# Optimization experiments

Measured on AMD Instinct MI355X. Metric: run time of the kernel, lower is better.

Reference implementation:

```python
import jax, jax.numpy as jnp
import numpy as np

N = 10000   # nodes (cells)
E = 100000  # edges
G = 2000    # num_genes
H = 20      # heads
C1 = 128    # layer-1 out channels per head
C2 = 128    # latent_dim
NEG_SLOPE = 0.2


def setup_inputs():
    key = jax.random.key(0)
    ks = jax.random.split(key, 9)
    s = 0.05
    return {
        "x": jax.random.normal(ks[0], (N, G), jnp.float32),
        "edge_index": jax.random.randint(ks[1], (2, E), 0, N, dtype=jnp.int64),
        "W1": jax.random.normal(ks[2], (G, H * C1), jnp.float32) * s,
        "att_src1": jax.random.normal(ks[3], (H, C1), jnp.float32) * s,
        "att_dst1": jax.random.normal(ks[4], (H, C1), jnp.float32) * s,
        "b1": jnp.zeros((H * C1,), jnp.float32),
        "W2": jax.random.normal(ks[5], (H * C1, H * C2), jnp.float32) * s,
        "att_src2": jax.random.normal(ks[6], (H, C2), jnp.float32) * s,
        "att_dst2": jax.random.normal(ks[7], (H, C2), jnp.float32) * s,
        "b2": jnp.zeros((C2,), jnp.float32),
    }


def _gat_conv(x, W, att_src, att_dst, bias, src, dst, concat):
    """PyG GATConv (eval mode, self-loops already in src/dst)."""
    n = x.shape[0]
    h_, c_ = att_src.shape
    h = (x @ W).reshape(n, h_, c_)                      # [N, H, C]
    a_src = jnp.einsum("nhc,hc->nh", h, att_src)        # [N, H]
    a_dst = jnp.einsum("nhc,hc->nh", h, att_dst)        # [N, H]
    e = a_src[src] + a_dst[dst]                          # [E, H]
    e = jnp.where(e > 0, e, NEG_SLOPE * e)               # leaky_relu
    # segment softmax over incoming edges of each destination node
    e_max = jax.ops.segment_max(e, dst, num_segments=n)  # [N, H]
    ex = jnp.exp(e - e_max[dst])                         # [E, H]
    denom = jax.ops.segment_sum(ex, dst, num_segments=n)
    alpha = ex / denom[dst]                              # [E, H]
    msg = alpha[:, :, None] * h[src]                     # [E, H, C]
    out = jax.ops.segment_sum(msg, dst, num_segments=n)  # [N, H, C]
    if concat:
        out = out.reshape(n, h_ * c_)
    else:
        out = out.mean(axis=1)                           # [N, C]
    return out + bias


def reference(x, edge_index, W1, att_src1, att_dst1, b1, W2, att_src2, att_dst2, b2):
    n = x.shape[0]
    loop = jnp.arange(n, dtype=edge_index.dtype)
    src = jnp.concatenate([edge_index[0], loop])  # PyG add_self_loops=True
    dst = jnp.concatenate([edge_index[1], loop])
    h1 = _gat_conv(x, W1, att_src1, att_dst1, b1, src, dst, concat=True)
    h1 = jax.nn.relu(h1)  # dropout is identity in eval mode
    h2 = _gat_conv(h1, W2, att_src2, att_dst2, b2, src, dst, concat=False)
    return jax.nn.relu(h2)
```

## Files before the change

### kernel.cpp

```cpp
#include <hip/hip_runtime.h>

#define NEG_SLOPE 0.2f

typedef __attribute__((ext_vector_type(4))) float floatx4;
typedef __attribute__((ext_vector_type(8))) short shortx8;

__device__ __forceinline__ unsigned short f2bf(float f) {
  union { float f; unsigned int u; } v;
  v.f = f;
  unsigned int r = (v.u + 0x7FFFu + ((v.u >> 16) & 1u)) >> 16;
  return (unsigned short)r;
}
__device__ __forceinline__ float bf2f(unsigned short u) {
  union { unsigned int u; float f; } v;
  v.u = (unsigned int)u << 16;
  return v.f;
}
__device__ __forceinline__ void store_out(float* p, float v) { *p = v; }
__device__ __forceinline__ void store_out(unsigned short* p, float v) { *p = f2bf(v); }

__device__ __forceinline__ void gload_lds16(const unsigned short* g, unsigned short* l) {
  __builtin_amdgcn_global_load_lds(
      (const __attribute__((address_space(1))) void*)(g),
      (__attribute__((address_space(3))) void*)(l), 16, 0, 0);
}

__device__ __forceinline__ int load_edge(const void* ei, long idx, int is64) {
  if (is64) return (int)((const long long*)ei)[idx];
  return ((const int*)ei)[idx];
}

__global__ void detect64_kernel(const unsigned int* __restrict__ p, int* __restrict__ flag) {
  int is64 = 1;
  for (int i = 0; i < 32; ++i)
    if (p[2 * i + 1] != 0u) is64 = 0;
  *flag = is64;
}

__global__ void init_cnt_kernel(int* __restrict__ cnt, int n) {
  int i = blockIdx.x * blockDim.x + threadIdx.x;
  if (i < n) cnt[i] = 1;
}

__global__ void count_kernel(const void* __restrict__ ei, const int* __restrict__ flag, int E,
                             int* __restrict__ cnt) {
  int e = blockIdx.x * blockDim.x + threadIdx.x;
  if (e >= E) return;
  int is64 = *flag;
  int d = load_edge(ei, (long)E + e, is64);
  atomicAdd(&cnt[d], 1);
}

__global__ __launch_bounds__(1024) void scan_kernel(const int* __restrict__ cnt,
                                                    int* __restrict__ offs, int n) {
  __shared__ int partial[1024];
  int t = threadIdx.x;
  int per = (n + 1023) / 1024;
  int beg = t * per;
  int end = min(beg + per, n);
  int sum = 0;
  for (int i = beg; i < end; ++i) sum += cnt[i];
  partial[t] = sum;
  __syncthreads();
  for (int d = 1; d < 1024; d <<= 1) {
    int v = (t >= d) ? partial[t - d] : 0;
    __syncthreads();
    partial[t] += v;
    __syncthreads();
  }
  int excl = (t == 0) ? 0 : partial[t - 1];
  for (int i = beg; i < end; ++i) { offs[i] = excl; excl += cnt[i]; }
  if (t == 1023) offs[n] = partial[1023];
}

__global__ void init_self_kernel(const int* __restrict__ offs, int* __restrict__ srcs,
                                 int* __restrict__ fill, int n) {
  int i = blockIdx.x * blockDim.x + threadIdx.x;
  if (i < n) { srcs[offs[i]] = i; fill[i] = 1; }
}

__global__ void scatter_kernel(const void* __restrict__ ei, const int* __restrict__ flag, int E,
                               const int* __restrict__ offs, int* __restrict__ fill,
                               int* __restrict__ srcs) {
  int e = blockIdx.x * blockDim.x + threadIdx.x;
  if (e >= E) return;
  int is64 = *flag;
  int s = load_edge(ei, e, is64);
  int d = load_edge(ei, (long)E + e, is64);
  int pos = offs[d] + atomicAdd(&fill[d], 1);
  srcs[pos] = s;
}


__global__ __launch_bounds__(256) void pack_a_kernel(const float* __restrict__ in,
                                                     unsigned short* __restrict__ out, int M,
                                                     int K, int Kpad) {
  int rt = blockIdx.x;
  int r = threadIdx.x & 127;
  int kq = threadIdx.x >> 7;
  int row = rt * 128 + r;
  int nkc = Kpad >> 3;
  unsigned short* obase = out + (long)rt * Kpad * 128 + r * 8;
  const float* irow = in + (long)row * K;
  for (int kc = kq + (int)blockIdx.y * 2; kc < nkc; kc += (int)gridDim.y * 2) {
    int k = kc << 3;
    shortx8 o;
    if (row < M && k + 8 <= K && (K & 3) == 0) {
      float4 v0 = *(const float4*)(irow + k);
      float4 v1 = *(const float4*)(irow + k + 4);
      o[0] = (short)f2bf(v0.x); o[1] = (short)f2bf(v0.y);
      o[2] = (short)f2bf(v0.z); o[3] = (short)f2bf(v0.w);
      o[4] = (short)f2bf(v1.x); o[5] = (short)f2bf(v1.y);
      o[6] = (short)f2bf(v1.z); o[7] = (short)f2bf(v1.w);
    } else {
#pragma unroll
      for (int i = 0; i < 8; ++i) {
        int kk = k + i;
        float v = (row < M && kk < K) ? irow[kk] : 0.f;
        o[i] = (short)f2bf(v);
      }
    }
    *(shortx8*)(obase + (long)kc * 1024) = o;
  }
}

__global__ __launch_bounds__(256) void transpose_pack_kernel(const float* __restrict__ in,
                                                             unsigned short* __restrict__ out,
                                                             int K, int N, int Kpad) {
  __shared__ float tile[32][33];
  int kb = blockIdx.x * 32;
  int nb = blockIdx.y * 32;
  int tx = threadIdx.x & 31;
  int ty = threadIdx.x >> 5;
#pragma unroll
  for (int i = 0; i < 32; i += 8) {
    int k = kb + ty + i;
    tile[ty + i][tx] = (k < K) ? in[(long)k * N + nb + tx] : 0.f;
  }
  __syncthreads();
  if (threadIdx.x < 128) {
    int nl = threadIdx.x & 31;
    int nn = nb + nl;
    int kc4 = threadIdx.x >> 5;
    int k0 = kc4 * 8;
    shortx8 o;
#pragma unroll
    for (int j = 0; j < 8; ++j) o[j] = (short)f2bf(tile[k0 + j][nl]);
    int kc = (kb >> 3) + kc4;
    *(shortx8*)(out + (long)(nn >> 7) * Kpad * 128 + (long)kc * 1024 + (nn & 127) * 8) = o;
  }
}

template <typename OT>
__global__ __launch_bounds__(256) void mfma_gemm_kernel(const unsigned short* __restrict__ A,
                                                        const unsigned short* __restrict__ Bt,
                                                        OT* __restrict__ C, int M, int N, int K) {
  __shared__ unsigned short As[3][4096];
  __shared__ unsigned short Bs[3][4096];

  int tid = threadIdx.x;
  int lane = tid & 63;
  int w = tid >> 6;
  int wm = w & 1, wn = w >> 1;
  int bn = blockIdx.x * 128;
  int bm = blockIdx.y * 128;
  int quad = lane >> 4, l16 = lane & 15;

  const unsigned short* pA = A + (long)(bm >> 7) * K * 128 + tid * 8;
  const unsigned short* pB = Bt + (long)(bn >> 7) * K * 128 + tid * 8;
  unsigned short* la = &As[0][0] + w * 512;
  unsigned short* lb = &Bs[0][0] + w * 512;

  floatx4 acc[4][4];
#pragma unroll
  for (int i = 0; i < 4; ++i)
#pragma unroll
    for (int j = 0; j < 4; ++j) acc[i][j] = (floatx4){0.f, 0.f, 0.f, 0.f};

  int nk = K >> 5;
  gload_lds16(pA, la);
  gload_lds16(pA + 2048, la + 2048);
  gload_lds16(pB, lb);
  gload_lds16(pB + 2048, lb + 2048);
  if (nk > 1) {
    gload_lds16(pA + 4096, la + 4096);
    gload_lds16(pA + 4096 + 2048, la + 4096 + 2048);
    gload_lds16(pB + 4096, lb + 4096);
    gload_lds16(pB + 4096 + 2048, lb + 4096 + 2048);
  }

  int cur = 0, st = 2;
  for (int k = 0; k < nk; ++k) {
    if (k + 2 < nk) {
      const unsigned short* qA = pA + (long)(k + 2) * 4096;
      const unsigned short* qB = pB + (long)(k + 2) * 4096;
      unsigned short* da = la + st * 4096;
      unsigned short* db = lb + st * 4096;
      gload_lds16(qA, da);
      gload_lds16(qA + 2048, da + 2048);
      gload_lds16(qB, db);
      gload_lds16(qB + 2048, db + 2048);
      __builtin_amdgcn_s_waitcnt(0x0F78);
    } else if (k + 1 < nk) {
      __builtin_amdgcn_s_waitcnt(0x0F74);
    } else {
      __builtin_amdgcn_s_waitcnt(0x0F70);
    }
    __builtin_amdgcn_s_barrier();

    shortx8 a[4], b[4];
#pragma unroll
    for (int i = 0; i < 4; ++i) {
      a[i] = *(const shortx8*)(&As[cur][(quad * 128 + wm * 64 + i * 16 + l16) * 8]);
      b[i] = *(const shortx8*)(&Bs[cur][(quad * 128 + wn * 64 + i * 16 + l16) * 8]);
    }
#pragma unroll
    for (int i = 0; i < 4; ++i)
#pragma unroll
      for (int j = 0; j < 4; ++j)
        acc[i][j] = __builtin_amdgcn_mfma_f32_16x16x32_bf16(a[i], b[j], acc[i][j], 0, 0, 0);

    __builtin_amdgcn_s_barrier();
    cur = (cur == 2) ? 0 : cur + 1;
    st = (st == 2) ? 0 : st + 1;
  }

  int orow0 = bm + wm * 64 + quad * 4;
  int ocol0 = bn + wn * 64 + l16;
#pragma unroll
  for (int i = 0; i < 4; ++i)
#pragma unroll
    for (int j = 0; j < 4; ++j)
#pragma unroll
      for (int r2 = 0; r2 < 4; ++r2) {
        int rr = orow0 + i * 16 + r2;
        if (rr < M) store_out(&C[(long)rr * N + ocol0 + j * 16], acc[i][j][r2]);
      }
}

__global__ __launch_bounds__(256) void att_coef_kernel(const unsigned short* __restrict__ h,
                                                       const float* __restrict__ att_s,
                                                       const float* __restrict__ att_d,
                                                       float* __restrict__ a_s,
                                                       float* __restrict__ a_d, int n, int H,
                                                       int C) {
  int wave = (int)((blockIdx.x * blockDim.x + threadIdx.x) >> 6);
  int lane = threadIdx.x & 63;
  if (wave >= n) return;
  const unsigned short* row = h + (long)wave * H * C;
  for (int hh = 0; hh < H; ++hh) {
    float s = 0.f, d = 0.f;
    for (int c = lane; c < C; c += 64) {
      float v = bf2f(row[hh * C + c]);
      s += v * att_s[hh * C + c];
      d += v * att_d[hh * C + c];
    }
#pragma unroll
    for (int o = 32; o > 0; o >>= 1) {
      s += __shfl_down(s, o, 64);
      d += __shfl_down(d, o, 64);
    }
    if (lane == 0) {
      a_s[(long)wave * H + hh] = s;
      a_d[(long)wave * H + hh] = d;
    }
  }
}

__global__ void edge_softmax_kernel(const float* __restrict__ a_src,
                                    const float* __restrict__ a_dst,
                                    const int* __restrict__ offs, const int* __restrict__ srcs,
                                    float* __restrict__ alpha, int n, int H) {
  int idx = blockIdx.x * blockDim.x + threadIdx.x;
  if (idx >= n * H) return;
  int dstn = idx / H;
  int hh = idx - dstn * H;
  int beg = offs[dstn], end = offs[dstn + 1];
  float ad = a_dst[idx];
  float m = -1e30f;
  for (int j = beg; j < end; ++j) {
    float e = a_src[srcs[j] * H + hh] + ad;
    e = e > 0.f ? e : NEG_SLOPE * e;
    m = fmaxf(m, e);
  }
  float ssum = 0.f;
  for (int j = beg; j < end; ++j) {
    float e = a_src[srcs[j] * H + hh] + ad;
    e = e > 0.f ? e : NEG_SLOPE * e;
    float ex = __expf(e - m);
    alpha[(long)j * H + hh] = ex;
    ssum += ex;
  }
  float inv = 1.f / ssum;
  for (int j = beg; j < end; ++j) alpha[(long)j * H + hh] *= inv;
}

__global__ __launch_bounds__(320) void aggregate1_kernel(const unsigned short* __restrict__ h,
                                                         const float* __restrict__ alpha,
                                                         const int* __restrict__ offs,
                                                         const int* __restrict__ srcs,
                                                         const float* __restrict__ bias,
                                                         unsigned short* __restrict__ out, int H,
                                                         int C, int HC) {
  int dstn = blockIdx.x;
  int t = threadIdx.x;
  int beg = offs[dstn], end = offs[dstn + 1];
  int nf8 = HC >> 3;
  for (int fid = t; fid < nf8; fid += blockDim.x) {
    int hh = (fid << 3) / C;
    float acc[8];
#pragma unroll
    for (int i = 0; i < 8; ++i) acc[i] = 0.f;
    for (int j = beg; j < end; ++j) {
      int s = srcs[j];
      float al = alpha[(long)j * H + hh];
      shortx8 r = ((const shortx8*)(h + (long)s * HC))[fid];
#pragma unroll
      for (int i = 0; i < 8; ++i) acc[i] = fmaf(al, bf2f((unsigned short)r[i]), acc[i]);
    }
    shortx8 o;
#pragma unroll
    for (int i = 0; i < 8; ++i) {
      float bb = bias[(fid << 3) + i];
      o[i] = (short)f2bf(fmaxf(acc[i] + bb, 0.f));
    }
    *(shortx8*)(out + (long)(dstn >> 7) * HC * 128 + (long)fid * 1024 + (dstn & 127) * 8) = o;
  }
}

__global__ __launch_bounds__(256) void aggregate2_kernel(const unsigned short* __restrict__ h,
                                                         const float* __restrict__ alpha,
                                                         const int* __restrict__ offs,
                                                         const int* __restrict__ srcs,
                                                         const float* __restrict__ bias,
                                                         float* __restrict__ out, int H, int C) {
  __shared__ float smem[16 * 256];
  int dstn = blockIdx.x;
  int t = threadIdx.x;
  int HC = H * C;
  int nc8 = C >> 3;
  int c8 = t & (nc8 - 1);
  int hgrp = t >> __builtin_ctz(nc8);
  int nHgrp = 256 >> __builtin_ctz(nc8);
  int beg = offs[dstn], end = offs[dstn + 1];

  float acc[2][8];
#pragma unroll
  for (int hi = 0; hi < 2; ++hi)
#pragma unroll
    for (int i = 0; i < 8; ++i) acc[hi][i] = 0.f;

  for (int j = beg; j < end; ++j) {
    int s = srcs[j];
    const unsigned short* row = h + (long)s * HC;
    const float* al = alpha + (long)j * H;
#pragma unroll
    for (int hi = 0; hi < 2; ++hi) {
      int hh = hgrp + hi * nHgrp;
      if (hh < H) {
        float a = al[hh];
        shortx8 r = *(const shortx8*)(row + hh * C + c8 * 8);
#pragma unroll
        for (int i = 0; i < 8; ++i) acc[hi][i] = fmaf(a, bf2f((unsigned short)r[i]), acc[hi][i]);
      }
    }
  }
#pragma unroll
  for (int i = 0; i < 8; ++i) smem[hgrp * C + c8 * 8 + i] = acc[0][i] + acc[1][i];
  __syncthreads();
  float invH = 1.f / (float)H;
  for (int c = t; c < C; c += 256) {
    float s = 0.f;
    for (int g = 0; g < nHgrp; ++g) s += smem[g * C + c];
    float v = s * invH + bias[c];
    out[(long)dstn * C + c] = v > 0.f ? v : 0.f;
  }
}

static inline size_t align256(size_t x) { return (x + 255) & ~(size_t)255; }

extern "C" void kernel_launch(void* const* d_in, const int* in_sizes, int n_in, void* d_out,
                              int out_size, void* d_ws, size_t ws_size, hipStream_t stream) {
  const float* x        = (const float*)d_in[0];
  const void*  ei       = d_in[1];
  const float* W1       = (const float*)d_in[2];
  const float* att_src1 = (const float*)d_in[3];
  const float* att_dst1 = (const float*)d_in[4];
  const float* b1       = (const float*)d_in[5];
  const float* W2       = (const float*)d_in[6];
  const float* att_src2 = (const float*)d_in[7];
  const float* att_dst2 = (const float*)d_in[8];
  const float* b2       = (const float*)d_in[9];
  float* out = (float*)d_out;

  const int C2  = in_sizes[9];
  const int H   = in_sizes[7] / C2;
  const int HC1 = in_sizes[5];
  const int C1  = HC1 / H;
  const int G   = in_sizes[2] / HC1;
  const int Nn  = in_sizes[0] / G;
  const int E   = in_sizes[1] / 2;
  const int HC2 = H * C2;
  const int Et  = E + Nn;
  const int Mpad = ((Nn + 127) / 128) * 128;
  const int K1pad = ((G + 31) / 32) * 32;

  char* p = (char*)d_ws;
  size_t off = 0;
  unsigned short* hb  = (unsigned short*)(p + off); off = align256(off + (size_t)Mpad * (HC1 > HC2 ? HC1 : HC2) * 2);
  unsigned short* xb  = (unsigned short*)(p + off); off = align256(off + (size_t)Mpad * K1pad * 2);
  unsigned short* xb2 = (unsigned short*)(p + off); off = align256(off + (size_t)Mpad * HC1 * 2);
  unsigned short* W1t = (unsigned short*)(p + off); off = align256(off + (size_t)HC1 * K1pad * 2);
  unsigned short* W2t = (unsigned short*)(p + off); off = align256(off + (size_t)HC2 * HC1 * 2);
  float* a_s   = (float*)(p + off); off = align256(off + (size_t)Nn * H * 4);
  float* a_d   = (float*)(p + off); off = align256(off + (size_t)Nn * H * 4);
  float* alpha = (float*)(p + off); off = align256(off + (size_t)Et * H * 4);
  int* cnt     = (int*)(p + off); off = align256(off + (size_t)Nn * 4);
  int* offs    = (int*)(p + off); off = align256(off + (size_t)(Nn + 1) * 4);
  int* fill    = (int*)(p + off); off = align256(off + (size_t)Nn * 4);
  int* srcs    = (int*)(p + off); off = align256(off + (size_t)Et * 4);
  int* flag64  = (int*)(p + off); off = align256(off + 16);
  (void)ws_size; (void)n_in; (void)out_size;

  const int TB = 256;
  detect64_kernel<<<1, 1, 0, stream>>>((const unsigned int*)ei, flag64);
  init_cnt_kernel<<<(Nn + TB - 1) / TB, TB, 0, stream>>>(cnt, Nn);
  count_kernel<<<(E + TB - 1) / TB, TB, 0, stream>>>(ei, flag64, E, cnt);
  scan_kernel<<<1, 1024, 0, stream>>>(cnt, offs, Nn);
  init_self_kernel<<<(Nn + TB - 1) / TB, TB, 0, stream>>>(offs, srcs, fill, Nn);
  scatter_kernel<<<(E + TB - 1) / TB, TB, 0, stream>>>(ei, flag64, E, offs, fill, srcs);

  {
    dim3 ga(Mpad / 128, 8);
    pack_a_kernel<<<ga, 256, 0, stream>>>(x, xb, Nn, G, K1pad);
    dim3 g1(K1pad / 32, HC1 / 32);
    transpose_pack_kernel<<<g1, 256, 0, stream>>>(W1, W1t, G, HC1, K1pad);
    dim3 g2(HC1 / 32, HC2 / 32);
    transpose_pack_kernel<<<g2, 256, 0, stream>>>(W2, W2t, HC1, HC2, HC1);
  }

  {
    dim3 grid(HC1 / 128, Mpad / 128);
    mfma_gemm_kernel<unsigned short><<<grid, 256, 0, stream>>>(xb, W1t, hb, Nn, HC1, K1pad);
  }
  att_coef_kernel<<<(Nn + 3) / 4, 256, 0, stream>>>(hb, att_src1, att_dst1, a_s, a_d, Nn, H, C1);
  edge_softmax_kernel<<<(Nn * H + TB - 1) / TB, TB, 0, stream>>>(a_s, a_d, offs, srcs, alpha, Nn, H);
  aggregate1_kernel<<<Nn, 320, 0, stream>>>(hb, alpha, offs, srcs, b1, xb2, H, C1, HC1);

  {
    dim3 grid(HC2 / 128, Mpad / 128);
    mfma_gemm_kernel<unsigned short><<<grid, 256, 0, stream>>>(xb2, W2t, hb, Nn, HC2, HC1);
  }
  att_coef_kernel<<<(Nn + 3) / 4, 256, 0, stream>>>(hb, att_src2, att_dst2, a_s, a_d, Nn, H, C2);
  edge_softmax_kernel<<<(Nn * H + TB - 1) / TB, TB, 0, stream>>>(a_s, a_d, offs, srcs, alpha, Nn, H);
  aggregate2_kernel<<<Nn, 256, 0, stream>>>(hb, alpha, offs, srcs, b2, out, H, C2);
}
```

Measured before the change: 869.5 us.

## Enlarge GEMM block tile to 256x256 with 8 waves and double buffering

New measurement: 879.5 us. No clear change (+1.1%).

```diff
diff --git a/kernel.cpp b/kernel.cpp
--- a/kernel.cpp
+++ b/kernel.cpp
@@ -152,83 +152,77 @@
 }
 
 template <typename OT>
-__global__ __launch_bounds__(256) void mfma_gemm_kernel(const unsigned short* __restrict__ A,
+__global__ __launch_bounds__(512) void mfma_gemm_kernel(const unsigned short* __restrict__ A,
                                                         const unsigned short* __restrict__ Bt,
                                                         OT* __restrict__ C, int M, int N, int K) {
-  __shared__ unsigned short As[3][4096];
-  __shared__ unsigned short Bs[3][4096];
+  __shared__ unsigned short As[2][8192];
+  __shared__ unsigned short Bs[2][8192];
 
   int tid = threadIdx.x;
   int lane = tid & 63;
   int w = tid >> 6;
-  int wm = w & 1, wn = w >> 1;
-  int bn = blockIdx.x * 128;
-  int bm = blockIdx.y * 128;
+  int wm = w >> 2, wn = w & 3;
+  int bn = blockIdx.x * 256;
+  int bm = blockIdx.y * 256;
   int quad = lane >> 4, l16 = lane & 15;
 
-  const unsigned short* pA = A + (long)(bm >> 7) * K * 128 + tid * 8;
-  const unsigned short* pB = Bt + (long)(bn >> 7) * K * 128 + tid * 8;
+  const unsigned short* pA0 = A + (long)(bm >> 7) * K * 128 + tid * 8;
+  const unsigned short* pA1 = pA0 + (long)K * 128;
+  const unsigned short* pB0 = Bt + (long)(bn >> 7) * K * 128 + tid * 8;
+  const unsigned short* pB1 = pB0 + (long)K * 128;
   unsigned short* la = &As[0][0] + w * 512;
   unsigned short* lb = &Bs[0][0] + w * 512;
 
-  floatx4 acc[4][4];
-#pragma unroll
-  for (int i = 0; i < 4; ++i)
+  floatx4 acc[8][4];
+#pragma unroll
+  for (int i = 0; i < 8; ++i)
 #pragma unroll
     for (int j = 0; j < 4; ++j) acc[i][j] = (floatx4){0.f, 0.f, 0.f, 0.f};
 
+  gload_lds16(pA0, la);
+  gload_lds16(pA1, la + 4096);
+  gload_lds16(pB0, lb);
+  gload_lds16(pB1, lb + 4096);
+
   int nk = K >> 5;
-  gload_lds16(pA, la);
-  gload_lds16(pA + 2048, la + 2048);
-  gload_lds16(pB, lb);
-  gload_lds16(pB + 2048, lb + 2048);
-  if (nk > 1) {
-    gload_lds16(pA + 4096, la + 4096);
-    gload_lds16(pA + 4096 + 2048, la + 4096 + 2048);
-    gload_lds16(pB + 4096, lb + 4096);
-    gload_lds16(pB + 4096 + 2048, lb + 4096 + 2048);
-  }
-
-  int cur = 0, st = 2;
   for (int k = 0; k < nk; ++k) {
-    if (k + 2 < nk) {
-      const unsigned short* qA = pA + (long)(k + 2) * 4096;
-      const unsigned short* qB = pB + (long)(k + 2) * 4096;
-      unsigned short* da = la + st * 4096;
-      unsigned short* db = lb + st * 4096;
-      gload_lds16(qA, da);
-      gload_lds16(qA + 2048, da + 2048);
-      gload_lds16(qB, db);
-      gload_lds16(qB + 2048, db + 2048);
-      __builtin_amdgcn_s_waitcnt(0x0F78);
-    } else if (k + 1 < nk) {
+    int cur = k & 1;
+    if (k + 1 < nk) {
+      long o = (long)(k + 1) * 4096;
+      unsigned short* da = la + (cur ^ 1) * 8192;
+      unsigned short* db = lb + (cur ^ 1) * 8192;
+      gload_lds16(pA0 + o, da);
+      gload_lds16(pA1 + o, da + 4096);
+      gload_lds16(pB0 + o, db);
+      gload_lds16(pB1 + o, db + 4096);
       __builtin_amdgcn_s_waitcnt(0x0F74);
     } else {
       __builtin_amdgcn_s_waitcnt(0x0F70);
     }
     __builtin_amdgcn_s_barrier();
 
-    shortx8 a[4], b[4];
-#pragma unroll
-    for (int i = 0; i < 4; ++i) {
-      a[i] = *(const shortx8*)(&As[cur][(quad * 128 + wm * 64 + i * 16 + l16) * 8]);
-      b[i] = *(const shortx8*)(&Bs[cur][(quad * 128 + wn * 64 + i * 16 + l16) * 8]);
-    }
-#pragma unroll
-    for (int i = 0; i < 4; ++i)
+    shortx8 b[4];
+#pragma unroll
+    for (int j = 0; j < 4; ++j) {
+      int c = wn * 64 + j * 16 + l16;
+      b[j] = *(const shortx8*)(&Bs[cur][(c >> 7) * 4096 + quad * 1024 + (c & 127) * 8]);
+    }
+#pragma unroll
+    for (int i = 0; i < 8; ++i) {
+      int r = i * 16 + l16;
+      shortx8 a = *(const shortx8*)(&As[cur][wm * 4096 + quad * 1024 + r * 8]);
 #pragma unroll
       for (int j = 0; j < 4; ++j)
-        acc[i][j] = __builtin_amdgcn_mfma_f32_16x16x32_bf16(a[i], b[j], acc[i][j], 0, 0, 0);
+        acc[i][j] = __builtin_amdgcn_mfma_f32_16x16x32_bf16(a, b[j], acc[i][j], 0, 0, 0);
+    }
 
     __builtin_amdgcn_s_barrier();
-    cur = (cur == 2) ? 0 : cur + 1;
-    st = (st == 2) ? 0 : st + 1;
-  }
-
-  int orow0 = bm + wm * 64 + quad * 4;
+  }
+
+  int orow0 = bm + wm * 128 + quad * 4;
   int ocol0 = bn + wn * 64 + l16;
 #pragma unroll
-  for (int i = 0; i < 4; ++i)
+  for (int i = 0; i < 8; ++i)
 #pragma unroll
     for (int j = 0; j < 4; ++j)
 #pragma unroll
@@ -402,7 +396,7 @@
   const int E   = in_sizes[1] / 2;
   const int HC2 = H * C2;
   const int Et  = E + Nn;
-  const int Mpad = ((Nn + 127) / 128) * 128;
+  const int Mpad = ((Nn + 255) / 256) * 256;
   const int K1pad = ((G + 31) / 32) * 32;
 
   char* p = (char*)d_ws;
@@ -440,16 +434,16 @@
   }
 
   {
-    dim3 grid(HC1 / 128, Mpad / 128);
-    mfma_gemm_kernel<unsigned short><<<grid, 256, 0, stream>>>(xb, W1t, hb, Nn, HC1, K1pad);
+    dim3 grid(HC1 / 256, Mpad / 256);
+    mfma_gemm_kernel<unsigned short><<<grid, 512, 0, stream>>>(xb, W1t, hb, Nn, HC1, K1pad);
   }
   att_coef_kernel<<<(Nn + 3) / 4, 256, 0, stream>>>(hb, att_src1, att_dst1, a_s, a_d, Nn, H, C1);
   edge_softmax_kernel<<<(Nn * H + TB - 1) / TB, TB, 0, stream>>>(a_s, a_d, offs, srcs, alpha, Nn, H);
   aggregate1_kernel<<<Nn, 320, 0, stream>>>(hb, alpha, offs, srcs, b1, xb2, H, C1, HC1);
 
   {
-    dim3 grid(HC2 / 128, Mpad / 128);
-    mfma_gemm_kernel<unsigned short><<<grid, 256, 0, stream>>>(xb2, W2t, hb, Nn, HC2, HC1);
+    dim3 grid(HC2 / 256, Mpad / 256);
+    mfma_gemm_kernel<unsigned short><<<grid, 512, 0, stream>>>(xb2, W2t, hb, Nn, HC2, HC1);
   }
   att_coef_kernel<<<(Nn + 3) / 4, 256, 0, stream>>>(hb, att_src2, att_dst2, a_s, a_d, Nn, H, C2);
   edge_softmax_kernel<<<(Nn * H + TB - 1) / TB, TB, 0, stream>>>(a_s, a_d, offs, srcs, alpha, Nn, H);
```
